# Performance work log

Measured on AMD Instinct MI355X. Metric: run time of the kernel, lower is better.

The kernel has to match this reference:

```python
import math
import jax, jax.numpy as jnp
import numpy as np

N_HEAD = 16
N_EMBD = 1024
HEAD_DIM = N_EMBD // N_HEAD  # 64
SHARED = 16
PRIV = HEAD_DIM - SHARED     # 48
B, T = 4, 2048
STD = 0.02


def setup_inputs() -> dict:
    key = jax.random.key(0)
    ks = jax.random.split(key, 6)
    x = jax.random.normal(ks[0], (B, T, N_EMBD), dtype=jnp.float32)
    # Linear params stored as (in, out); bias zeros per _reset_parameters
    W_share = jax.random.normal(ks[1], (N_EMBD, SHARED), dtype=jnp.float32) * STD
    Wq = jax.random.normal(ks[2], (N_EMBD, N_HEAD * PRIV), dtype=jnp.float32) * STD
    Wk = jax.random.normal(ks[3], (N_EMBD, N_HEAD * PRIV), dtype=jnp.float32) * STD
    Wv = jax.random.normal(ks[4], (N_EMBD, N_EMBD), dtype=jnp.float32) * STD
    Wo = jax.random.normal(ks[5], (N_EMBD, N_EMBD), dtype=jnp.float32) * STD
    return {
        'hidden_states': x,
        'W_share': W_share, 'b_share': jnp.zeros((SHARED,), jnp.float32),
        'Wq': Wq, 'bq': jnp.zeros((N_HEAD * PRIV,), jnp.float32),
        'Wk': Wk, 'bk': jnp.zeros((N_HEAD * PRIV,), jnp.float32),
        'Wv': Wv, 'bv': jnp.zeros((N_EMBD,), jnp.float32),
        'Wo': Wo, 'bo': jnp.zeros((N_EMBD,), jnp.float32),
    }


def reference(hidden_states, W_share, b_share, Wq, bq, Wk, bk, Wv, bv, Wo, bo):
    x = hidden_states
    Bt, Tt, C = x.shape
    # shared projection, broadcast across heads: (B,T,s) -> (B,H,T,s)
    share = x @ W_share + b_share
    share_h = jnp.broadcast_to(share[:, None, :, :], (Bt, N_HEAD, Tt, SHARED))
    # private q/k: (B,T,H*p) -> (B,H,T,p)
    q_priv = (x @ Wq + bq).reshape(Bt, Tt, N_HEAD, PRIV).transpose(0, 2, 1, 3)
    k_priv = (x @ Wk + bk).reshape(Bt, Tt, N_HEAD, PRIV).transpose(0, 2, 1, 3)
    q = jnp.concatenate([share_h, q_priv], axis=-1)  # (B,H,T,head_dim)
    k = jnp.concatenate([share_h, k_priv], axis=-1)
    v = (x @ Wv + bv).reshape(Bt, Tt, N_HEAD, HEAD_DIM).transpose(0, 2, 1, 3)
    scale = 1.0 / math.sqrt(HEAD_DIM)
    att = jnp.einsum('bhqd,bhkd->bhqk', q, k) * scale
    causal = jnp.tril(jnp.ones((Tt, Tt), dtype=bool))
    att = jnp.where(causal[None, None, :, :], att, -jnp.inf)
    att = jax.nn.softmax(att, axis=-1)
    y = jnp.einsum('bhqk,bhkd->bhqd', att, v)
    y = y.transpose(0, 2, 1, 3).reshape(Bt, Tt, C)
    y = y @ Wo + bo
    return y
```

## Files before the change

kernel.cpp:

```cpp
#include <hip/hip_runtime.h>
#include <hip/hip_bf16.h>

typedef unsigned short u16;
typedef short short8 __attribute__((ext_vector_type(8)));
typedef float f32x4 __attribute__((ext_vector_type(4)));
typedef float f32x16 __attribute__((ext_vector_type(16)));
typedef unsigned uint32x4 __attribute__((ext_vector_type(4)));

#define N_EMBD   1024
#define N_HEADS  16
#define HEAD_DIM 64
#define PRIV     48
#define SEQ_T    2048
#define BATCH    4
#define M_ROWS   (BATCH*SEQ_T)
#define PNS      2816
#define QOFF     64
#define KOFF     832
#define VOFF     1600
#define NTILES   (SEQ_T/64)
#define NT_K     16

#if __has_builtin(__builtin_amdgcn_exp2f)
#define EXP2(x) __builtin_amdgcn_exp2f(x)
#else
#define EXP2(x) exp2f(x)
#endif

#if __has_builtin(__builtin_amdgcn_global_load_lds)
#define HAVE_GLL 1
#else
#define HAVE_GLL 0
#endif

#if __has_builtin(__builtin_amdgcn_permlane32_swap)
#define HAVE_PLSWAP 1
typedef unsigned uint2v __attribute__((ext_vector_type(2)));
#else
#define HAVE_PLSWAP 0
#endif

__device__ __forceinline__ u16 f2bf(float f) {
  __hip_bfloat16 h = __float2bfloat16(f);
  return *reinterpret_cast<u16*>(&h);
}
__device__ __forceinline__ float bf2f(u16 s) {
  __hip_bfloat16 h;
  *reinterpret_cast<u16*>(&h) = s;
  return __bfloat162float(h);
}
__device__ __forceinline__ float loadv(const void* p, size_t i, int isf32) {
  return isf32 ? ((const float*)p)[i] : bf2f(((const u16*)p)[i]);
}
__device__ __forceinline__ u16 truncbf(float f) {
  unsigned u = __builtin_bit_cast(unsigned, f);
  return (u16)(u >> 16);
}
#if HAVE_GLL
__device__ __forceinline__ void gload_lds16(const u16* g, u16* l) {
  __builtin_amdgcn_global_load_lds(
      (const __attribute__((address_space(1))) void*)g,
      (__attribute__((address_space(3))) void*)l, 16, 0, 0);
}
#endif

__global__ __launch_bounds__(256) void detect_kernel(const u16* __restrict__ x,
                                                     int* __restrict__ flag) {
  __shared__ int cnt;
  if (threadIdx.x == 0) cnt = 0;
  __syncthreads();
  u16 v = x[2 * threadIdx.x];
  int e = (v >> 7) & 0xFF;
  int junk = (e >= 0xC0 || (e != 0 && e <= 0x30)) ? 1 : 0;
  if (junk) atomicAdd(&cnt, 1);
  __syncthreads();
  if (threadIdx.x == 0) *flag = (cnt > 16) ? 1 : 0;
}

__global__ __launch_bounds__(256) void pack_t_kernel(
    const void* __restrict__ Wsh, const void* __restrict__ Wq,
    const void* __restrict__ Wk,  const void* __restrict__ Wv,
    const void* __restrict__ Wo,
    const void* __restrict__ bsh, const void* __restrict__ bq,
    const void* __restrict__ bk,  const void* __restrict__ bv,
    const void* __restrict__ bo,
    u16* __restrict__ Wcat, u16* __restrict__ Woc,
    u16* __restrict__ bcat, u16* __restrict__ boc,
    const void* __restrict__ x, u16* __restrict__ Xb,
    const int* __restrict__ flagp)
{
  const int f = *flagp;
  if (blockIdx.z == 6) {
    const int flat = blockIdx.y * 16 + blockIdx.x;
#pragma unroll
    for (int it = 0; it < 16; it++) {
      size_t i = (size_t)flat * 4096 + it * 256 + threadIdx.x;
      if (f) {
        const float4* p = (const float4*)x;
        float4 a = p[i * 2], b = p[i * 2 + 1];
        u16 t[8] = {f2bf(a.x), f2bf(a.y), f2bf(a.z), f2bf(a.w),
                    f2bf(b.x), f2bf(b.y), f2bf(b.z), f2bf(b.w)};
        *(uint4*)&Xb[i * 8] = *(const uint4*)t;
      } else {
        *(uint4*)&Xb[i * 8] = ((const uint4*)x)[i];
      }
    }
    return;
  }
  if (blockIdx.z == 5) {
    const int flat = blockIdx.y * 16 + blockIdx.x;
    const int padRows = 48 + 192;
    for (int i = flat * 256 + threadIdx.x; i < padRows * 1024; i += 256 * 256) {
      int r = i >> 10, c2 = i & 1023;
      int row = (r < 48) ? (16 + r) : (2624 + (r - 48));
      Wcat[(size_t)row * 1024 + c2] = 0;
    }
    if (flat == 0) {
      for (int c = threadIdx.x; c < PNS; c += 256) {
        float v = 0.f;
        if (c < 16)         v = loadv(bsh, c, f);
        else if (c < QOFF)  v = 0.f;
        else if (c < KOFF)  v = loadv(bq, c - QOFF, f);
        else if (c < VOFF)  v = loadv(bk, c - KOFF, f);
        else if (c < 2624)  v = loadv(bv, c - VOFF, f);
        bcat[c] = f2bf(v);
      }
    } else if (flat == 1) {
      for (int c = threadIdx.x; c < N_EMBD; c += 256)
        boc[c] = f2bf(loadv(bo, c, f));
    }
    return;
  }
  const void* src; u16* dst; int N, rowOff;
  switch (blockIdx.z) {
    case 0: src = Wsh; dst = Wcat; N = 16;   rowOff = 0;    break;
    case 1: src = Wq;  dst = Wcat; N = 768;  rowOff = QOFF; break;
    case 2: src = Wk;  dst = Wcat; N = 768;  rowOff = KOFF; break;
    case 3: src = Wv;  dst = Wcat; N = 1024; rowOff = VOFF; break;
    default:src = Wo;  dst = Woc;  N = 1024; rowOff = 0;    break;
  }
  const int n0 = blockIdx.x * 64;
  if (n0 >= N) return;
  const int k0 = blockIdx.y * 64;
  __shared__ u16 t[64][65];
  const int tx = threadIdx.x & 63, ty = threadIdx.x >> 6;
#pragma unroll
  for (int rr = 0; rr < 16; rr++) {
    int k = k0 + ty * 16 + rr;
    int n = n0 + tx;
    float v = (n < N) ? loadv(src, (size_t)k * N + n, f) : 0.f;
    t[ty * 16 + rr][tx] = f2bf(v);
  }
  __syncthreads();
#pragma unroll
  for (int rr = 0; rr < 16; rr++) {
    int n = ty * 16 + rr;
    if (n0 + n < N)
      dst[(size_t)(rowOff + n0 + n) * 1024 + k0 + tx] = t[tx][n];
  }
}

__global__ __launch_bounds__(512, 2) void gemm8p_kernel(
    const u16* __restrict__ A,
    const u16* __restrict__ Bt,
    const u16* __restrict__ bias,
    void* __restrict__ C, int ldc, int Mtiles,
    const int* __restrict__ flagp, int c_dyn,
    u16* __restrict__ VtOut, int vt_en)
{
  (void)Mtiles;
  __shared__ __align__(16) u16 smem[73728];
  u16* const As = smem;
  u16* const Bs = smem + 3 * 8192;

  const bool cf32 = (c_dyn != 0) && (*flagp != 0);

  const int tid  = threadIdx.x;
  const int lane = tid & 63;
  const int w    = tid >> 6;
  const int quad = lane >> 4, l16 = lane & 15;
  const int wm   = w >> 2, wn = w & 3;

  const int xcd = blockIdx.x & 7;
  const int s   = blockIdx.x >> 3;
  const int mb  = xcd * 8 + (s & 7);
  const int nb  = s >> 3;
  const int m0  = mb * 128, n0 = nb * 256;

  int ldsA[2]; size_t glA[2];
  int ldsB[2][2]; size_t glB[2][2];
#pragma unroll
  for (int rd = 0; rd < 2; rd++) {
    int j = tid + rd * 512, rp = j >> 3, sl = j & 7;
    int cl = (sl ^ (rp & 7)) * 8;
    ldsA[rd] = rp * 64 + sl * 8;
    glA[rd]  = (size_t)(m0 + rp) * 1024 + cl;
#pragma unroll
    for (int nh = 0; nh < 2; nh++) {
      int cc = (rp & 31) + nh * 32 + (rp >> 5) * 64;
      ldsB[nh][rd] = cc * 64 + sl * 8;
      glB[nh][rd]  = (size_t)(n0 + cc) * 1024 + cl;
    }
  }

#if HAVE_GLL
#define G8(g, l) gload_lds16((g), (l))
#else
#define G8(g, l) (*(uint4*)(l) = *(const uint4*)(g))
#endif
#define STG_A(t, bf)                                                       \
  if ((t) < NT_K) {                                                        \
    _Pragma("unroll") for (int rd = 0; rd < 2; rd++)                       \
      G8(A + glA[rd] + (t) * 64, As + (bf) * 8192 + ldsA[rd]);             \
  }
#define STG_B(nh, t, bf)                                                   \
  if ((t) < NT_K) {                                                        \
    _Pragma("unroll") for (int rd = 0; rd < 2; rd++)                       \
      G8(Bt + glB[nh][rd] + (t) * 64, Bs + (bf) * 16384 + ldsB[nh][rd]);   \
  }

  const int ck0  = ((quad)     ^ (l16 & 7)) * 8;
  const int ck1  = ((4 + quad) ^ (l16 & 7)) * 8;
  const int arow = (wm * 64 + l16) * 64;
  const int brow = (wn * 64 + l16) * 64;

  f32x4 acc[4][4];
#pragma unroll
  for (int i = 0; i < 4; i++)
#pragma unroll
    for (int j = 0; j < 4; j++) acc[i][j] = (f32x4){0.f, 0.f, 0.f, 0.f};

  short8 af[4][2], bA[2][2], bB[2][2];

#define READ_A(cur)                                                        \
  { const u16* pa = As + (cur) * 8192 + arow;                              \
    _Pragma("unroll") for (int m = 0; m < 4; m++) {                        \
      af[m][0] = *(const short8*)(pa + m * 1024 + ck0);                    \
      af[m][1] = *(const short8*)(pa + m * 1024 + ck1); } }
#define READ_B(dst, nh, cur)                                               \
  { const u16* pb = Bs + (cur) * 16384 + brow + (nh) * 2048;               \
    _Pragma("unroll") for (int n = 0; n < 2; n++) {                        \
      dst[n][0] = *(const short8*)(pb + n * 1024 + ck0);                   \
      dst[n][1] = *(const short8*)(pb + n * 1024 + ck1); } }
#define MM16(bfr, nh)                                                      \
  __builtin_amdgcn_s_setprio(1);                                           \
  _Pragma("unroll") for (int m = 0; m < 4; m++)                            \
    _Pragma("unroll") for (int n = 0; n < 2; n++) {                        \
      acc[m][(nh)*2+n] = __builtin_amdgcn_mfma_f32_16x16x32_bf16(          \
          af[m][0], bfr[n][0], acc[m][(nh)*2+n], 0, 0, 0);                 \
      acc[m][(nh)*2+n] = __builtin_amdgcn_mfma_f32_16x16x32_bf16(          \
          af[m][1], bfr[n][1], acc[m][(nh)*2+n], 0, 0, 0); }               \
  __builtin_amdgcn_s_setprio(0);
#define BARR { __builtin_amdgcn_s_barrier(); __builtin_amdgcn_sched_barrier(0); }

  STG_A(0, 0); STG_B(1, 0, 0); STG_B(0, 0, 0);
  STG_A(1, 1); STG_B(1, 1, 1); STG_B(0, 1, 1);
  asm volatile("s_waitcnt vmcnt(6)");
  BARR;

#pragma unroll
  for (int kt = 0; kt < NT_K; kt++) {
    const int cur = kt % 3;
    const int stb = (kt + 2) % 3;
    READ_A(cur); READ_B(bA, 0, cur);
    STG_A(kt + 2, stb); STG_B(1, kt + 2, stb);
    BARR;
    MM16(bA, 0);
    BARR;
    READ_B(bB, 1, cur);
    STG_B(0, kt + 2, stb);
    BARR;
    MM16(bB, 1);
    if (kt < NT_K - 2)       { asm volatile("s_waitcnt vmcnt(6)"); }
    else if (kt == NT_K - 2) { asm volatile("s_waitcnt vmcnt(0)"); }
    BARR;
  }
#undef STG_A
#undef STG_B
#undef READ_A
#undef READ_B
#undef MM16
#undef BARR
#undef G8

  __syncthreads();

  float bvv[4];
#pragma unroll
  for (int ni = 0; ni < 4; ni++)
    bvv[ni] = bf2f(bias[n0 + wn * 64 + ni * 16 + l16]);

  const int ncol0 = n0 + wn * 64;
  if (vt_en && ncol0 >= VOFF && ncol0 < VOFF + 1024) {
    u16* cs = smem + w * 4096;
#pragma unroll
    for (int m = 0; m < 4; m++)
#pragma unroll
      for (int ni = 0; ni < 4; ni++)
#pragma unroll
        for (int r = 0; r < 4; r++) {
          int d  = ni * 16 + l16;
          int tc = m * 2 + (quad >> 1);
          int te = (quad & 1) * 4 + r;
          cs[d * 64 + ((tc ^ (d & 7)) * 8) + te] = f2bf(acc[m][ni][r] + bvv[ni]);
        }
    const int bb = (m0 + wm * 64) >> 11;
    const int t0 = (m0 + wm * 64) & 2047;
    const int hh = (ncol0 - VOFF) >> 6;
    __builtin_amdgcn_s_barrier();
#pragma unroll
    for (int i = 0; i < 8; i++) {
      int ch = lane + i * 64;
      int rr = ch >> 3, cc = ch & 7;
      short8 v = *(const short8*)(cs + rr * 64 + ((cc ^ (rr & 7)) * 8));
      *(short8*)&VtOut[((size_t)(bb * 16 + hh) * 64 + rr) * SEQ_T + t0 + cc * 8] = v;
    }
  } else if (!cf32) {
    u16* cs = smem + w * 4096;
#pragma unroll
    for (int m = 0; m < 4; m++)
#pragma unroll
      for (int ni = 0; ni < 4; ni++)
#pragma unroll
        for (int r = 0; r < 4; r++) {
          int row = m * 16 + quad * 4 + r;
          int ch  = ((ni * 2 + (l16 >> 3)) ^ (row & 7)) * 8 + (l16 & 7);
          cs[row * 64 + ch] = f2bf(acc[m][ni][r] + bvv[ni]);
        }
    u16* Cb = (u16*)C;
#pragma unroll
    for (int i = 0; i < 8; i++) {
      int ch = lane + i * 64;
      int rr = ch >> 3, cc = ch & 7;
      short8 v = *(const short8*)(cs + rr * 64 + ((cc ^ (rr & 7)) * 8));
      *(short8*)&Cb[(size_t)(m0 + wm * 64 + rr) * ldc + n0 + wn * 64 + cc * 8] = v;
    }
  } else {
    float* cf = (float*)(void*)smem + w * 2048;
#pragma unroll
    for (int pass = 0; pass < 2; pass++) {
#pragma unroll
      for (int m2 = 0; m2 < 2; m2++)
#pragma unroll
        for (int ni = 0; ni < 4; ni++)
#pragma unroll
          for (int r = 0; r < 4; r++) {
            int row = m2 * 16 + quad * 4 + r;
            int ch  = ((ni * 4 + (l16 >> 2)) ^ (row & 15)) * 4 + (l16 & 3);
            cf[row * 64 + ch] = acc[pass * 2 + m2][ni][r] + bvv[ni];
          }
      float* Cf = (float*)C;
#pragma unroll
      for (int i = 0; i < 8; i++) {
        int ch = lane + i * 64;
        int rr = ch >> 4, cc = ch & 15;
        f32x4 v = *(const f32x4*)(cf + rr * 64 + ((cc ^ (rr & 15)) * 4));
        *(f32x4*)&Cf[(size_t)(m0 + wm * 64 + pass * 32 + rr) * ldc +
                     n0 + wn * 64 + cc * 4] = v;
      }
    }
  }
}

__global__ __launch_bounds__(256, 3) void attn_kernel(
    const u16* __restrict__ P, const u16* __restrict__ Vt,
    u16* __restrict__ Y)
{
  const int bh  = blockIdx.x;
  const int b   = bh >> 4, h = bh & 15;
  const int j   = 15 - blockIdx.y;
  const int qtA = 2 * j, qtB = 2 * j + 1;
  const int tid = threadIdx.x;
  const int w   = tid >> 6;
  const int lane = tid & 63;
  const int l32 = lane & 31, hi = lane >> 5;
  const size_t rowb = (size_t)b * SEQ_T;
  const int qcol = QOFF + h * PRIV;
  const int kcol = KOFF + h * PRIV;

  __shared__ __align__(16) u16 Ks[3][64 * 64];
  __shared__ __align__(16) u16 Vs[3][64 * 64];

  const float csc = 0.18033688011112042f;
  const int iA = qtA * 64 + w * 16, iB = qtB * 64 + w * 16;
  const int gi = (l32 < 16) ? (iA + l32) : (iB + l32 - 16);
  const u16* qptr = P + (rowb + gi) * PNS;

  short8 qb[4];
  qb[0] = *(const short8*)&qptr[8 * hi];
#pragma unroll
  for (int c = 1; c < 4; c++)
    qb[c] = *(const short8*)&qptr[qcol + 16 * c + 8 * hi - 16];
#pragma unroll
  for (int c = 0; c < 4; c++)
#pragma unroll
    for (int e = 0; e < 8; e++)
      qb[c][e] = (short)f2bf(bf2f((u16)qb[c][e]) * csc);

  short8 ones;
#pragma unroll
  for (int e = 0; e < 8; e++) ones[e] = (short)0x3F80;

  const int nkt = qtB + 1;

#if HAVE_GLL
#define GLOADA(g, l) gload_lds16((g), (l))
#else
#define GLOADA(g, l) (*(uint4*)(l) = *(const uint4*)(g))
#endif
#define STAGE_KV(t, bb)                                                        \
  {                                                                            \
    const int kk0 = (t) * 64;                                                  \
    _Pragma("unroll") for (int i2 = 0; i2 < 2; i2++) {                         \
      int c   = tid + i2 * 256;                                                \
      int row = c >> 3;                                                        \
      int dg  = ((c & 7) ^ (row & 7)) * 8;                                     \
      int col = (dg < 16) ? dg : (kcol + dg - 16);                             \
      GLOADA(&P[(rowb + kk0 + row) * PNS + col], &Ks[bb][c * 8]);              \
      GLOADA(&Vt[((size_t)bh * 64 + row) * SEQ_T + kk0 + dg], &Vs[bb][c * 8]); \
    }                                                                          \
  }

  f32x16 accy[2], accl;
#pragma unroll
  for (int r = 0; r < 16; r++) { accy[0][r] = 0.f; accy[1][r] = 0.f; accl[r] = 0.f; }

  const float ninf = -__builtin_inff();

  STAGE_KV(0, 0);
  STAGE_KV(1, 1);
  asm volatile("s_waitcnt vmcnt(4)" ::: "memory");
  __builtin_amdgcn_sched_barrier(0);
  __builtin_amdgcn_s_barrier();

  for (int kt = 0; kt < nkt; kt++) {
    const int cur = kt % 3;
    const int k0  = kt * 64;
    if (kt + 2 < nkt) STAGE_KV(kt + 2, (kt + 2) % 3);

#pragma unroll
    for (int kk = 0; kk < 2; kk++) {
      f32x16 s;
#pragma unroll
      for (int r = 0; r < 16; r++) s[r] = 0.f;
      const int krow = kk * 32 + l32;
      __builtin_amdgcn_s_setprio(1);
#pragma unroll
      for (int c = 0; c < 4; c++) {
        short8 ka = *(const short8*)&Ks[cur][krow * 64 + (((2 * c + hi) ^ (krow & 7)) * 8)];
        s = __builtin_amdgcn_mfma_f32_32x32x16_bf16(ka, qb[c], s, 0, 0, 0);
      }
      __builtin_amdgcn_s_setprio(0);

      if (kt == qtA || kt == qtB) {
#pragma unroll
        for (int r = 0; r < 16; r++) {
          int gj = k0 + kk * 32 + (r & 3) + 8 * (r >> 2) + 4 * hi;
          if (gj > gi) s[r] = ninf;
        }
      }
      if (kt > qtA) {
#pragma unroll
        for (int r = 0; r < 16; r++)
          if (l32 < 16) s[r] = ninf;
      }

      float px[16];
#pragma unroll
      for (int r = 0; r < 16; r++) px[r] = EXP2(s[r]);

#pragma unroll
      for (int kc = 0; kc < 2; kc++) {
        unsigned g0, g1, g2, g3;
        asm("v_cvt_pk_bf16_f32 %0, %1, %2" : "=v"(g0) : "v"(px[8*kc+0]), "v"(px[8*kc+1]));
        asm("v_cvt_pk_bf16_f32 %0, %1, %2" : "=v"(g1) : "v"(px[8*kc+2]), "v"(px[8*kc+3]));
        asm("v_cvt_pk_bf16_f32 %0, %1, %2" : "=v"(g2) : "v"(px[8*kc+4]), "v"(px[8*kc+5]));
        asm("v_cvt_pk_bf16_f32 %0, %1, %2" : "=v"(g3) : "v"(px[8*kc+6]), "v"(px[8*kc+7]));
#if HAVE_PLSWAP
        uint2v r02 = __builtin_amdgcn_permlane32_swap(g0, g2, false, false);
        uint2v r13 = __builtin_amdgcn_permlane32_swap(g1, g3, false, false);
        uint32x4 pv = {r02.x, r13.x, r02.y, r13.y};
#else
        unsigned a0 = g0, b0 = g2, a1 = g1, b1 = g3;
        asm("v_permlane32_swap_b32 %0, %1" : "+v"(a0), "+v"(b0));
        asm("v_permlane32_swap_b32 %0, %1" : "+v"(a1), "+v"(b1));
        uint32x4 pv = {a0, a1, b0, b1};
#endif
        short8 pa = __builtin_bit_cast(short8, pv);

        __builtin_amdgcn_s_setprio(1);
        accl = __builtin_amdgcn_mfma_f32_32x32x16_bf16(pa, ones, accl, 0, 0, 0);
#pragma unroll
        for (int dt = 0; dt < 2; dt++) {
          int vrow = dt * 32 + l32;
          short8 vbf = *(const short8*)&Vs[cur][vrow * 64 + (((4*kk + 2*kc + hi) ^ (vrow & 7)) * 8)];
          accy[dt] = __builtin_amdgcn_mfma_f32_32x32x16_bf16(pa, vbf, accy[dt], 0, 0, 0);
        }
        __builtin_amdgcn_s_setprio(0);
      }
    }

    if (kt + 3 < nkt) {
      asm volatile("s_waitcnt vmcnt(4)" ::: "memory");
      __builtin_amdgcn_sched_barrier(0);
      __builtin_amdgcn_s_barrier();
    } else if (kt + 2 == nkt) {
      asm volatile("s_waitcnt vmcnt(0)" ::: "memory");
      __builtin_amdgcn_sched_barrier(0);
      __builtin_amdgcn_s_barrier();
    } else if (kt + 3 == nkt) {
      asm volatile("s_waitcnt vmcnt(4)" ::: "memory");
      __builtin_amdgcn_sched_barrier(0);
      __builtin_amdgcn_s_barrier();
    }
  }
#undef STAGE_KV
#undef GLOADA

  float inv[16];
#pragma unroll
  for (int r = 0; r < 16; r++) inv[r] = 1.0f / accl[r];
#pragma unroll
  for (int r = 0; r < 16; r++) {
    int q = (r & 3) + 8 * (r >> 2) + 4 * hi;
    int grow = (r < 8) ? (iA + q) : (iB + q - 16);
    size_t base = (rowb + grow) * N_EMBD + h * HEAD_DIM + l32;
    Y[base]      = f2bf(accy[0][r] * inv[r]);
    Y[base + 32] = f2bf(accy[1][r] * inv[r]);
  }
}

extern "C" void kernel_launch(void* const* d_in, const int* in_sizes, int n_in,
                              void* d_out, int out_size, void* d_ws, size_t ws_size,
                              hipStream_t stream) {
  (void)in_sizes; (void)n_in; (void)out_size; (void)ws_size;
  const void* x   = d_in[0];
  const void* Wsh = d_in[1];
  const void* bsh = d_in[2];
  const void* Wq  = d_in[3];
  const void* bq  = d_in[4];
  const void* Wk  = d_in[5];
  const void* bk  = d_in[6];
  const void* Wv  = d_in[7];
  const void* bv  = d_in[8];
  const void* Wo  = d_in[9];
  const void* bo  = d_in[10];

  char* wsb = (char*)d_ws;
  int* flag = (int*)wsb;
  u16* ws16 = (u16*)(wsb + 64);
  u16* Wcat = ws16;
  u16* bcat = Wcat + (size_t)PNS * N_EMBD;
  u16* Woc  = bcat + PNS;
  u16* boc  = Woc + (size_t)N_EMBD * N_EMBD;
  u16* Pb   = boc + N_EMBD;
  u16* Yb   = Pb + (size_t)M_ROWS * PNS;
  u16* Vtb  = Yb + (size_t)M_ROWS * N_EMBD;
  u16* Xb   = Yb;

  detect_kernel<<<dim3(1), dim3(256), 0, stream>>>((const u16*)x, flag);
  pack_t_kernel<<<dim3(16, 16, 7), dim3(256), 0, stream>>>(
      Wsh, Wq, Wk, Wv, Wo, bsh, bq, bk, bv, bo, Wcat, Woc, bcat, boc,
      x, Xb, flag);
  gemm8p_kernel<<<dim3(64 * (PNS / 256)), dim3(512), 0, stream>>>(
      Xb, Wcat, bcat, Pb, PNS, 64, flag, 0, Vtb, 1);
  attn_kernel<<<dim3(BATCH * N_HEADS, NTILES / 2), dim3(256), 0, stream>>>(
      Pb, Vtb, Yb);
  gemm8p_kernel<<<dim3(64 * (N_EMBD / 256)), dim3(512), 0, stream>>>(
      Yb, Woc, boc, d_out, N_EMBD, 64, flag, 1, nullptr, 0);
}
```

Baseline: 258.2 us.

## Fuse dtype detection into pack kernel, drop V-transpose duplicate store, replace ones-MFMA rowsum

Moves the input-dtype detection into every block of the pack kernel, removing a separate single-block launch, and has one block write the flag for later kernels. The QKV GEMM now returns early for tiles past the V columns when the transposed-V path is enabled, so it skips storing P columns no later kernel reads. In attention, the softmax denominator is no longer an extra MFMA against a ones matrix per step; it becomes a per-lane scalar sum of the exponentials, combined across half-waves with a shuffle and broadcast per row at the end. This trades matrix-unit work for VALU adds and shuffles, and the sum is now taken in fp32 before bf16 rounding, which shifts numerics slightly.

Measured after the change: 247.8 us. 4.0% less time.

```diff
diff --git a/kernel.cpp b/kernel.cpp
--- a/kernel.cpp
+++ b/kernel.cpp
@@ -64,19 +64,6 @@
 }
 #endif
 
-__global__ __launch_bounds__(256) void detect_kernel(const u16* __restrict__ x,
-                                                     int* __restrict__ flag) {
-  __shared__ int cnt;
-  if (threadIdx.x == 0) cnt = 0;
-  __syncthreads();
-  u16 v = x[2 * threadIdx.x];
-  int e = (v >> 7) & 0xFF;
-  int junk = (e >= 0xC0 || (e != 0 && e <= 0x30)) ? 1 : 0;
-  if (junk) atomicAdd(&cnt, 1);
-  __syncthreads();
-  if (threadIdx.x == 0) *flag = (cnt > 16) ? 1 : 0;
-}
-
 __global__ __launch_bounds__(256) void pack_t_kernel(
     const void* __restrict__ Wsh, const void* __restrict__ Wq,
     const void* __restrict__ Wk,  const void* __restrict__ Wv,
@@ -87,9 +74,19 @@
     u16* __restrict__ Wcat, u16* __restrict__ Woc,
     u16* __restrict__ bcat, u16* __restrict__ boc,
     const void* __restrict__ x, u16* __restrict__ Xb,
-    const int* __restrict__ flagp)
+    int* __restrict__ flagp)
 {
-  const int f = *flagp;
+  __shared__ int cnt_sm;
+  if (threadIdx.x == 0) cnt_sm = 0;
+  __syncthreads();
+  {
+    u16 v = ((const u16*)x)[2 * threadIdx.x];
+    int e = (v >> 7) & 0xFF;
+    if (e >= 0xC0 || (e != 0 && e <= 0x30)) atomicAdd(&cnt_sm, 1);
+  }
+  __syncthreads();
+  const int f = (cnt_sm > 16) ? 1 : 0;
+
   if (blockIdx.z == 6) {
     const int flat = blockIdx.y * 16 + blockIdx.x;
 #pragma unroll
@@ -116,6 +113,7 @@
       Wcat[(size_t)row * 1024 + c2] = 0;
     }
     if (flat == 0) {
+      if (threadIdx.x == 0) *flagp = f;
       for (int c = threadIdx.x; c < PNS; c += 256) {
         float v = 0.f;
         if (c < 16)         v = loadv(bsh, c, f);
@@ -291,7 +289,8 @@
     bvv[ni] = bf2f(bias[n0 + wn * 64 + ni * 16 + l16]);
 
   const int ncol0 = n0 + wn * 64;
-  if (vt_en && ncol0 >= VOFF && ncol0 < VOFF + 1024) {
+  if (vt_en && ncol0 >= VOFF + 1024) return;
+  if (vt_en && ncol0 >= VOFF) {
     u16* cs = smem + w * 4096;
 #pragma unroll
     for (int m = 0; m < 4; m++)
@@ -397,10 +396,6 @@
     for (int e = 0; e < 8; e++)
       qb[c][e] = (short)f2bf(bf2f((u16)qb[c][e]) * csc);
 
-  short8 ones;
-#pragma unroll
-  for (int e = 0; e < 8; e++) ones[e] = (short)0x3F80;
-
   const int nkt = qtB + 1;
 
 #if HAVE_GLL
@@ -421,9 +416,10 @@
     }                                                                          \
   }
 
-  f32x16 accy[2], accl;
-#pragma unroll
-  for (int r = 0; r < 16; r++) { accy[0][r] = 0.f; accy[1][r] = 0.f; accl[r] = 0.f; }
+  f32x16 accy[2];
+#pragma unroll
+  for (int r = 0; r < 16; r++) { accy[0][r] = 0.f; accy[1][r] = 0.f; }
+  float vsum = 0.f;
 
   const float ninf = -__builtin_inff();
 
@@ -468,6 +464,10 @@
       float px[16];
 #pragma unroll
       for (int r = 0; r < 16; r++) px[r] = EXP2(s[r]);
+      vsum += (((px[0] + px[1]) + (px[2] + px[3])) +
+               ((px[4] + px[5]) + (px[6] + px[7]))) +
+              (((px[8] + px[9]) + (px[10] + px[11])) +
+               ((px[12] + px[13]) + (px[14] + px[15])));
 
 #pragma unroll
       for (int kc = 0; kc < 2; kc++) {
@@ -489,7 +489,6 @@
         short8 pa = __builtin_bit_cast(short8, pv);
 
         __builtin_amdgcn_s_setprio(1);
-        accl = __builtin_amdgcn_mfma_f32_32x32x16_bf16(pa, ones, accl, 0, 0, 0);
 #pragma unroll
         for (int dt = 0; dt < 2; dt++) {
           int vrow = dt * 32 + l32;
@@ -517,16 +516,16 @@
 #undef STAGE_KV
 #undef GLOADA
 
-  float inv[16];
-#pragma unroll
-  for (int r = 0; r < 16; r++) inv[r] = 1.0f / accl[r];
+  float tot  = vsum + __shfl_xor(vsum, 32);
+  float invq = 1.0f / tot;
 #pragma unroll
   for (int r = 0; r < 16; r++) {
     int q = (r & 3) + 8 * (r >> 2) + 4 * hi;
+    float iv = __shfl(invq, q);
     int grow = (r < 8) ? (iA + q) : (iB + q - 16);
     size_t base = (rowb + grow) * N_EMBD + h * HEAD_DIM + l32;
-    Y[base]      = f2bf(accy[0][r] * inv[r]);
-    Y[base + 32] = f2bf(accy[1][r] * inv[r]);
+    Y[base]      = f2bf(accy[0][r] * iv);
+    Y[base + 32] = f2bf(accy[1][r] * iv);
   }
 }
 
@@ -558,7 +557,6 @@
   u16* Vtb  = Yb + (size_t)M_ROWS * N_EMBD;
   u16* Xb   = Yb;
 
-  detect_kernel<<<dim3(1), dim3(256), 0, stream>>>((const u16*)x, flag);
   pack_t_kernel<<<dim3(16, 16, 7), dim3(256), 0, stream>>>(
       Wsh, Wq, Wk, Wv, Wo, bsh, bq, bk, bv, bo, Wcat, Woc, bcat, boc,
       x, Xb, flag);
```
